# Performance work log

Hardware: AMD Instinct MI355X
Metric: run time of the kernel (lower is better)

The kernel has to match this reference:

```python
import jax, jax.numpy as jnp
import numpy as np

# Static module config (from init_kwargs)
NX, NY, NZ = 360, 360, 1
C = 128  # NUM_BEV_FEATURES // NZ
B = 4    # batch size (coords[:,0].max()+1 in the original; static here)
N = 160000


def setup_inputs() -> dict:
    key = jax.random.key(0)
    k1, k2, k3, k4 = jax.random.split(key, 4)
    pillar_features = jax.random.normal(k1, (N, C), dtype=jnp.float32)
    b = jax.random.randint(k2, (N,), 0, B, dtype=jnp.int32)
    z = jnp.zeros((N,), dtype=jnp.int32)  # NZ == 1
    y = jax.random.randint(k3, (N,), 0, NY, dtype=jnp.int32)
    x = jax.random.randint(k4, (N,), 0, NX, dtype=jnp.int32)
    voxel_coords = jnp.stack([b, z, y, x], axis=1)  # [N, 4] (batch, z, y, x)
    return {"pillar_features": pillar_features, "voxel_coords": voxel_coords}


def reference(pillar_features, voxel_coords):
    S = NZ * NY * NX  # cells per sample
    c = voxel_coords.astype(jnp.int32)
    # fused batch + spatial index: b*S + z*ny*nx + y*nx + x
    gidx = c[:, 0] * S + c[:, 1] * (NY * NX) + c[:, 2] * NX + c[:, 3]
    sums = jax.ops.segment_sum(pillar_features, gidx, num_segments=B * S)  # [B*S, C]
    cnt = jax.ops.segment_sum(jnp.ones((pillar_features.shape[0],), pillar_features.dtype),
                              gidx, num_segments=B * S)                    # [B*S]
    mean = sums / jnp.maximum(cnt, 1.0)[:, None]  # scatter_mean: empty cells stay 0
    # [B*S, C] -> [B, S, C] -> [B, C, S] -> [B, C*NZ, NY, NX]
    bev = mean.reshape(B, S, C).transpose(0, 2, 1).reshape(B, C * NZ, NY, NX)
    return bev
```

## Files before the change

kernel.cpp:

```cpp
#include <hip/hip_runtime.h>


typedef float nfloat4 __attribute__((ext_vector_type(4)));

constexpr int NXc = 360;
constexpr int NYc = 360;
constexpr int NZc = 1;
constexpr int Cc  = 128;
constexpr int Bc  = 4;
constexpr int Sc  = NZc * NYc * NXc;
constexpr int BSc = Bc * Sc;

constexpr int TSC   = 540;
constexpr int NST   = BSc / TSC;
constexpr int CHG   = 16;
constexpr int NCG   = Cc / CHG;
constexpr int CAP3  = 240;
constexpr int LSTR  = TSC + 1;
constexpr int CSTRIDE = 16;

__global__ void pps_fill3(const int* __restrict__ coords,
                          int* __restrict__ cnt, int* __restrict__ list, int N) {
    int i = blockIdx.x * blockDim.x + threadIdx.x;
    if (i >= N) return;
    int4 c = reinterpret_cast<const int4*>(coords)[i];
    int g = c.x * Sc + c.y * (NYc * NXc) + c.z * NXc + c.w;
    int st = g / TSC;
    int cell = g - st * TSC;
    int slot = atomicAdd(&cnt[st * CSTRIDE], 1);
    if (slot < CAP3) list[st * CAP3 + slot] = (i << 10) | cell;
}

__global__ __launch_bounds__(512)
void pps_gather6(const float* __restrict__ feat,
                 const int* __restrict__ cnt,
                 const int* __restrict__ list,
                 float* __restrict__ out) {
    __shared__ __align__(16) float lsum[CHG * LSTR];
    __shared__ int   lcnt[TSC];
    __shared__ float linv[TSC];
    __shared__ int   slist[CAP3];
    __shared__ int   sm;

    const int st = blockIdx.x % NST;
    const int cg = blockIdx.x / NST;
    const int t  = threadIdx.x;

    for (int k = t; k < (CHG * LSTR) / 4; k += 512)
        reinterpret_cast<nfloat4*>(lsum)[k] = (nfloat4)0.0f;
    for (int k = t; k < TSC; k += 512) lcnt[k] = 0;
    if (t == 0) sm = min(cnt[st * CSTRIDE], CAP3);
    if (t < CAP3) slist[t] = list[st * CAP3 + t];
    __syncthreads();

    const int w = t >> 6, l = t & 63, psub = l >> 4, ch = l & 15;
    const int m = sm;
    #pragma unroll 2
    for (int sb = w * 4; sb < m; sb += 32) {
        int slot = sb + psub;
        bool ok = slot < m;
        int e = slist[ok ? slot : 0];
        int cell = e & 1023;
        int p = e >> 10;
        if (ok) {
            float v = feat[(size_t)p * Cc + cg * CHG + ch];
            atomicAdd(&lsum[ch * LSTR + cell], v);
            if (ch == 0) atomicAdd(&lcnt[cell], 1);
        }
    }
    __syncthreads();

    for (int k = t; k < TSC; k += 512) {
        int n = lcnt[k];
        linv[k] = n > 0 ? 1.0f / (float)n : 0.0f;
    }
    __syncthreads();

    const int b  = st / (Sc / TSC);
    const int s0 = (st % (Sc / TSC)) * TSC;
    float* ob = out + ((size_t)b * Cc + cg * CHG) * Sc + s0;
    #pragma unroll
    for (int i = 0; i < 17; ++i) {
        int idx = i * 512 + t;
        if (idx < CHG * TSC) {
            int cl  = idx / TSC;
            int pos = idx - cl * TSC;
            float val = lsum[cl * LSTR + pos] * linv[pos];
            __builtin_nontemporal_store(val, ob + (size_t)cl * Sc + pos);
        }
    }
}

__global__ void pps_count_kernel(const int* __restrict__ coords,
                                 int* __restrict__ cnt, int N) {
    int i = blockIdx.x * blockDim.x + threadIdx.x;
    if (i >= N) return;
    int4 c = reinterpret_cast<const int4*>(coords)[i];
    int gidx = c.x * Sc + c.y * (NYc * NXc) + c.z * NXc + c.w;
    atomicAdd(&cnt[gidx], 1);
}

__global__ void pps_scatter_kernel(const float* __restrict__ feat,
                                   const int* __restrict__ coords,
                                   const int* __restrict__ cnt,
                                   float* __restrict__ out, int N) {
    int t = blockIdx.x * blockDim.x + threadIdx.x;
    int i = t >> 5;
    int g = t & 31;
    if (i >= N) return;
    int4 c = reinterpret_cast<const int4*>(coords)[i];
    int s    = c.y * (NYc * NXc) + c.z * NXc + c.w;
    int gidx = c.x * Sc + s;
    int n = cnt[gidx];
    float4 v = reinterpret_cast<const float4*>(feat + (size_t)i * Cc)[g];
    float* base = out + ((size_t)c.x * Cc + (size_t)g * 4) * Sc + s;
    if (n == 1) {
        base[0 * (size_t)Sc] = v.x;
        base[1 * (size_t)Sc] = v.y;
        base[2 * (size_t)Sc] = v.z;
        base[3 * (size_t)Sc] = v.w;
    } else {
        float inv = 1.0f / (float)n;
        atomicAdd(&base[0 * (size_t)Sc], v.x * inv);
        atomicAdd(&base[1 * (size_t)Sc], v.y * inv);
        atomicAdd(&base[2 * (size_t)Sc], v.z * inv);
        atomicAdd(&base[3 * (size_t)Sc], v.w * inv);
    }
}

extern "C" void kernel_launch(void* const* d_in, const int* in_sizes, int n_in,
                              void* d_out, int out_size, void* d_ws, size_t ws_size,
                              hipStream_t stream) {
    const float* feat   = reinterpret_cast<const float*>(d_in[0]);
    const int*   coords = reinterpret_cast<const int*>(d_in[1]);
    float*       out    = reinterpret_cast<float*>(d_out);

    const int N = in_sizes[0] / Cc;

    const size_t cnt_bytes  = (size_t)NST * CSTRIDE * sizeof(int);
    const size_t list_bytes = (size_t)NST * CAP3 * sizeof(int);

    if (ws_size >= cnt_bytes + list_bytes) {
        int* cnt  = reinterpret_cast<int*>(d_ws);
        int* list = reinterpret_cast<int*>((char*)d_ws + cnt_bytes);
        (void)hipMemsetAsync(d_ws, 0, cnt_bytes, stream);
        {
            int threads = 256;
            int blocks = (N + threads - 1) / threads;
            pps_fill3<<<blocks, threads, 0, stream>>>(coords, cnt, list, N);
        }
        pps_gather6<<<NST * NCG, 512, 0, stream>>>(feat, cnt, list, out);
    } else {
        int* cnt = reinterpret_cast<int*>(d_ws);
        (void)hipMemsetAsync(d_out, 0, (size_t)out_size * sizeof(float), stream);
        (void)hipMemsetAsync(d_ws, 0, (size_t)BSc * sizeof(int), stream);
        {
            int threads = 256;
            int blocks = (N + threads - 1) / threads;
            pps_count_kernel<<<blocks, threads, 0, stream>>>(coords, cnt, N);
        }
        {
            int threads = 256;
            long long total = (long long)N * 32;
            int blocks = (int)((total + threads - 1) / threads);
            pps_scatter_kernel<<<blocks, threads, 0, stream>>>(feat, coords, cnt, out, N);
        }
    }
}
```

Before: 147.6 us.

## Precompute per-cell counts in fill pass and load gather features as float4 up front

```diff
diff --git a/kernel.cpp b/kernel.cpp
--- a/kernel.cpp
+++ b/kernel.cpp
@@ -19,60 +19,79 @@
 constexpr int LSTR  = TSC + 1;
 constexpr int CSTRIDE = 16;
 
-__global__ void pps_fill3(const int* __restrict__ coords,
-                          int* __restrict__ cnt, int* __restrict__ list, int N) {
+__global__ void pps_fill4(const int* __restrict__ coords,
+                          int* __restrict__ tcnt,
+                          int* __restrict__ cellcnt,
+                          int* __restrict__ list, int N) {
     int i = blockIdx.x * blockDim.x + threadIdx.x;
     if (i >= N) return;
     int4 c = reinterpret_cast<const int4*>(coords)[i];
     int g = c.x * Sc + c.y * (NYc * NXc) + c.z * NXc + c.w;
     int st = g / TSC;
     int cell = g - st * TSC;
-    int slot = atomicAdd(&cnt[st * CSTRIDE], 1);
+    int slot = atomicAdd(&tcnt[st * CSTRIDE], 1);
     if (slot < CAP3) list[st * CAP3 + slot] = (i << 10) | cell;
+    atomicAdd(&cellcnt[g], 1);
 }
 
 __global__ __launch_bounds__(512)
-void pps_gather6(const float* __restrict__ feat,
-                 const int* __restrict__ cnt,
+void pps_gather7(const float* __restrict__ feat,
+                 const int* __restrict__ tcnt,
+                 const int* __restrict__ cellcnt,
                  const int* __restrict__ list,
                  float* __restrict__ out) {
     __shared__ __align__(16) float lsum[CHG * LSTR];
-    __shared__ int   lcnt[TSC];
     __shared__ float linv[TSC];
-    __shared__ int   slist[CAP3];
-    __shared__ int   sm;
 
     const int st = blockIdx.x % NST;
     const int cg = blockIdx.x / NST;
     const int t  = threadIdx.x;
 
-    for (int k = t; k < (CHG * LSTR) / 4; k += 512)
-        reinterpret_cast<nfloat4*>(lsum)[k] = (nfloat4)0.0f;
-    for (int k = t; k < TSC; k += 512) lcnt[k] = 0;
-    if (t == 0) sm = min(cnt[st * CSTRIDE], CAP3);
-    if (t < CAP3) slist[t] = list[st * CAP3 + t];
-    __syncthreads();
+    #pragma unroll
+    for (int k = 0; k < 5; ++k) {
+        int idx = k * 512 + t;
+        if (idx < (CHG * LSTR) / 4)
+            reinterpret_cast<nfloat4*>(lsum)[idx] = (nfloat4)0.0f;
+    }
 
-    const int w = t >> 6, l = t & 63, psub = l >> 4, ch = l & 15;
-    const int m = sm;
-    #pragma unroll 2
-    for (int sb = w * 4; sb < m; sb += 32) {
-        int slot = sb + psub;
-        bool ok = slot < m;
-        int e = slist[ok ? slot : 0];
-        int cell = e & 1023;
-        int p = e >> 10;
-        if (ok) {
-            float v = feat[(size_t)p * Cc + cg * CHG + ch];
-            atomicAdd(&lsum[ch * LSTR + cell], v);
-            if (ch == 0) atomicAdd(&lcnt[cell], 1);
-        }
+    const int m = min(tcnt[st * CSTRIDE], CAP3);
+
+    const int w = t >> 6, l = t & 63;
+    const int psub = l >> 2;
+    const int cq   = l & 3;
+    const int s0i = w * 16 + psub;
+    const int s1i = s0i + 128;
+    const bool ok0 = s0i < m;
+    const bool ok1 = s1i < m;
+    const int base = st * CAP3;
+    int e0 = 0, e1 = 0;
+    if (ok0) e0 = list[base + s0i];
+    if (ok1) e1 = list[base + s1i];
+    nfloat4 v0, v1;
+    const float* fbase = feat + cg * CHG + cq * 4;
+    if (ok0) v0 = *reinterpret_cast<const nfloat4*>(fbase + (size_t)(e0 >> 10) * Cc);
+    if (ok1) v1 = *reinterpret_cast<const nfloat4*>(fbase + (size_t)(e1 >> 10) * Cc);
+
+    const int gbase = st * TSC;
+    for (int k = t; k < TSC; k += 512) {
+        int n = cellcnt[gbase + k];
+        linv[k] = n > 0 ? 1.0f / (float)n : 0.0f;
     }
     __syncthreads();
 
-    for (int k = t; k < TSC; k += 512) {
-        int n = lcnt[k];
-        linv[k] = n > 0 ? 1.0f / (float)n : 0.0f;
+    if (ok0) {
+        int c0 = e0 & 1023;
+        atomicAdd(&lsum[(cq * 4 + 0) * LSTR + c0], v0.x);
+        atomicAdd(&lsum[(cq * 4 + 1) * LSTR + c0], v0.y);
+        atomicAdd(&lsum[(cq * 4 + 2) * LSTR + c0], v0.z);
+        atomicAdd(&lsum[(cq * 4 + 3) * LSTR + c0], v0.w);
+    }
+    if (ok1) {
+        int c1 = e1 & 1023;
+        atomicAdd(&lsum[(cq * 4 + 0) * LSTR + c1], v1.x);
+        atomicAdd(&lsum[(cq * 4 + 1) * LSTR + c1], v1.y);
+        atomicAdd(&lsum[(cq * 4 + 2) * LSTR + c1], v1.z);
+        atomicAdd(&lsum[(cq * 4 + 3) * LSTR + c1], v1.w);
     }
     __syncthreads();
 
@@ -137,19 +156,21 @@
 
     const int N = in_sizes[0] / Cc;
 
-    const size_t cnt_bytes  = (size_t)NST * CSTRIDE * sizeof(int);
+    const size_t tcnt_bytes = (size_t)NST * CSTRIDE * sizeof(int);
+    const size_t cell_bytes = (size_t)BSc * sizeof(int);
     const size_t list_bytes = (size_t)NST * CAP3 * sizeof(int);
 
-    if (ws_size >= cnt_bytes + list_bytes) {
-        int* cnt  = reinterpret_cast<int*>(d_ws);
-        int* list = reinterpret_cast<int*>((char*)d_ws + cnt_bytes);
-        (void)hipMemsetAsync(d_ws, 0, cnt_bytes, stream);
+    if (ws_size >= tcnt_bytes + cell_bytes + list_bytes) {
+        int* tcnt    = reinterpret_cast<int*>(d_ws);
+        int* cellcnt = reinterpret_cast<int*>((char*)d_ws + tcnt_bytes);
+        int* list    = reinterpret_cast<int*>((char*)d_ws + tcnt_bytes + cell_bytes);
+        (void)hipMemsetAsync(d_ws, 0, tcnt_bytes + cell_bytes, stream);
         {
             int threads = 256;
             int blocks = (N + threads - 1) / threads;
-            pps_fill3<<<blocks, threads, 0, stream>>>(coords, cnt, list, N);
+            pps_fill4<<<blocks, threads, 0, stream>>>(coords, tcnt, cellcnt, list, N);
         }
-        pps_gather6<<<NST * NCG, 512, 0, stream>>>(feat, cnt, list, out);
+        pps_gather7<<<NST * NCG, 512, 0, stream>>>(feat, tcnt, cellcnt, list, out);
     } else {
         int* cnt = reinterpret_cast<int*>(d_ws);
         (void)hipMemsetAsync(d_out, 0, (size_t)out_size * sizeof(float), stream);
```

Result: slower. 157.4 us (+6.6%).
